# Optimization experiments

Measured on AMD Instinct MI355X. Metric: run time of the kernel, lower is better.

The kernel has to match this reference:

```python
import jax, jax.numpy as jnp
import numpy as np

B, T, D, H = 4, 4096, 1024, 16
DH = D // H
NB = T // 2 + 1  # rfft bins


def setup_inputs() -> dict:
    key = jax.random.key(0)
    ks = jax.random.split(key, 6)
    x = jax.random.normal(ks[0], (B, T, D), dtype=jnp.float32)
    # torch nn.Linear params: weight [out, in], bias [out]
    W_qkv = jax.random.normal(ks[1], (3 * D, D), dtype=jnp.float32) * 0.02
    b_qkv = jnp.zeros((3 * D,), dtype=jnp.float32)
    W_o = jax.random.normal(ks[2], (D, D), dtype=jnp.float32) * 0.02
    b_o = jnp.zeros((D,), dtype=jnp.float32)
    # per-head per-bin spectral filters (smart-init-like small values)
    log_gain = jax.random.normal(ks[3], (H, NB), dtype=jnp.float32) * 0.05
    phase = jax.random.normal(ks[4], (H, NB), dtype=jnp.float32) * 0.01
    return {"x": x, "W_qkv": W_qkv, "b_qkv": b_qkv, "W_o": W_o,
            "b_o": b_o, "log_gain": log_gain, "phase": phase}


def reference(x, W_qkv, b_qkv, W_o, b_o, log_gain, phase):
    # qkv projection; only v is used on the spectral path (q,k discarded)
    qkv = jnp.einsum('btd,ed->bte', x, W_qkv) + b_qkv  # [B,T,3D]
    v = qkv[..., 2 * D:]                               # [B,T,D]
    v = v.reshape(B, T, H, DH).transpose(0, 2, 1, 3)   # [B,H,T,DH]
    # rFFT along the token dim
    v_f = jnp.fft.rfft(v.astype(jnp.float32), axis=2)  # [B,H,NB,DH] complex
    # per-head per-bin complex filter: polar(exp(log_gain), phase)
    mag = jnp.exp(log_gain)
    comp = jax.lax.complex(mag * jnp.cos(phase), mag * jnp.sin(phase))  # [H,NB]
    v_f = v_f * comp[None, :, :, None]
    y_h = jnp.fft.irfft(v_f, n=T, axis=2)              # [B,H,T,DH]
    y = y_h.transpose(0, 2, 1, 3).reshape(B, T, D)     # [B,T,D]
    y = jnp.einsum('btd,ed->bte', y, W_o) + b_o
    return x + y
```

## Files before the change

kernel.cpp:

```cpp
#include <hip/hip_runtime.h>
#include <hip/hip_bf16.h>
#include <math.h>

#define B_BATCH 4
#define T_LEN   4096
#define D_DIM   1024
#define H_HEADS 16
#define NB_BINS 2049
#define M_ROWS  (B_BATCH * T_LEN)

typedef __attribute__((ext_vector_type(8))) short short8;
typedef __attribute__((ext_vector_type(8))) unsigned short u16x8;
typedef __attribute__((ext_vector_type(4))) float f32x4;

__device__ __forceinline__ ushort f2bf(float f) {
    unsigned b = __float_as_uint(f);
    unsigned r = (b + 0x7fffu + ((b >> 16) & 1u)) >> 16;
    return (ushort)r;
}
__device__ __forceinline__ float bf2f(ushort u) {
    return __uint_as_float(((unsigned)u) << 16);
}

__global__ void cvt_f32_to_bf16(const float* __restrict__ src, ushort* __restrict__ dst, int n4) {
    int i = blockIdx.x * 256 + threadIdx.x;
    if (i >= n4) return;
    float4 v = ((const float4*)src)[i];
    ushort4 o;
    o.x = f2bf(v.x); o.y = f2bf(v.y); o.z = f2bf(v.z); o.w = f2bf(v.w);
    ((ushort4*)dst)[i] = o;
}

__global__ void cvt_weights(const float* __restrict__ wv, const float* __restrict__ wo,
                            ushort* __restrict__ wvb, ushort* __restrict__ wob, int n4) {
    int i = blockIdx.x * 256 + threadIdx.x;
    const float* src = (i < n4) ? wv : wo;
    ushort* dst = (i < n4) ? wvb : wob;
    int j = (i < n4) ? i : (i - n4);
    float4 v = ((const float4*)src)[j];
    ushort4 o;
    o.x = f2bf(v.x); o.y = f2bf(v.y); o.z = f2bf(v.z); o.w = f2bf(v.w);
    ((ushort4*)dst)[j] = o;
}

__device__ __forceinline__ int drev16(int i) {
    return ((i & 15) << 8) | (i & 0xF0) | (i >> 8);
}

__global__ void prep_tables(const float* __restrict__ lg, const float* __restrict__ ph,
                            float2* __restrict__ Cdr, float2* __restrict__ tw) {
    int idx = blockIdx.x * 256 + threadIdx.x;
    if (idx < 4096) {
        double th = -2.0 * 3.14159265358979323846 * (double)idx / 4096.0;
        tw[idx] = make_float2((float)cos(th), (float)sin(th));
    }
    if (idx >= H_HEADS * 4096) return;
    int h = idx >> 12, i = idx & 4095;
    int f = drev16(i);
    int fc = (f <= 2048) ? f : (4096 - f);
    float sgn = (f <= 2048) ? 1.f : -1.f;
    float m = expf(lg[h * NB_BINS + fc]) * (1.0f / 4096.0f);
    float p = ph[h * NB_BINS + fc];
    float re = m * __cosf(p), im = sgn * m * __sinf(p);
    if (fc == 0 || fc == 2048) im = 0.f;
    Cdr[idx] = make_float2(re, im);
}

template<bool RESID, bool BIASROW>
__global__ __launch_bounds__(512, 1) void gemm256(const ushort* __restrict__ A,
        const ushort* __restrict__ Bm, const float* __restrict__ bias,
        const float* __restrict__ resid, void* __restrict__ Cout,
        int M, int N, int K) {
    __shared__ ushort lds[49152];
    const int tid  = threadIdx.x;
    const int lane = tid & 63;
    const int wid  = tid >> 6;
    const int wr   = wid >> 2, wc = wid & 3;
    const int fr   = lane & 15;
    const int nbn  = N >> 8;
    int bid = (int)blockIdx.x;
    bid = (bid & 7) * ((int)gridDim.x >> 3) + (bid >> 3);
    const int bm = bid / nbn, bn = bid % nbn;
    const int row0 = bm << 8, col0 = bn << 8;
    const int NT = K >> 5;

    f32x4 acc[8][4];
#pragma unroll
    for (int i = 0; i < 8; i++)
#pragma unroll
        for (int j = 0; j < 4; j++) acc[i][j] = (f32x4){0.f, 0.f, 0.f, 0.f};

    auto stage = [&](const ushort* P, int gr0, int k0, int lb) {
#pragma unroll
        for (int i = 0; i < 2; i++) {
            int r = (wid << 5) + (i << 4) + (lane >> 2);
            int c = ((lane & 3) ^ ((lane >> 3) & 3)) << 3;
            const ushort* g = P + (size_t)(gr0 + r) * (size_t)K + (size_t)(k0 + c);
            __builtin_amdgcn_global_load_lds(
                (const __attribute__((address_space(1))) void*)g,
                (__attribute__((address_space(3))) void*)&lds[lb + (((wid << 1) + i) << 9)],
                16, 0, 0);
        }
    };
    auto rdfrag = [&](int base, int row) -> short8 {
        int g = (((lane >> 4) ^ ((row >> 1) & 3)) << 3);
        return *(const short8*)&lds[base + (row << 5) + g];
    };

    stage(A,  row0, 0, 0);
    stage(Bm, col0, 0, 24576);
    stage(A,  row0, 32, 8192);
    stage(Bm, col0, 32, 24576 + 8192);
    asm volatile("s_waitcnt vmcnt(4)" ::: "memory");
    __builtin_amdgcn_sched_barrier(0);
    __builtin_amdgcn_s_barrier();

    short8 aF[4], bF[4];
    for (int t = 0; t < NT; ++t) {
        const int cb = (t % 3) << 13;
        const int sb = ((t + 2) % 3) << 13;
        const bool st = (t + 2) < NT;
        const int k2 = (t + 2) << 5;

#pragma unroll
        for (int mi = 0; mi < 4; mi++) aF[mi] = rdfrag(cb, (wr << 7) + (mi << 4) + fr);
#pragma unroll
        for (int ni = 0; ni < 4; ni++) bF[ni] = rdfrag(24576 + cb, (wc << 6) + (ni << 4) + fr);
        if (st) stage(A, row0, k2, sb);
        __builtin_amdgcn_s_barrier();
        asm volatile("s_waitcnt lgkmcnt(0)" ::: "memory");
        __builtin_amdgcn_sched_barrier(0);
        __builtin_amdgcn_s_setprio(1);
#pragma unroll
        for (int mi = 0; mi < 4; mi++)
#pragma unroll
            for (int ni = 0; ni < 4; ni++)
                acc[mi][ni] = __builtin_amdgcn_mfma_f32_16x16x32_bf16(aF[mi], bF[ni], acc[mi][ni], 0, 0, 0);
        __builtin_amdgcn_s_setprio(0);
        __builtin_amdgcn_sched_barrier(0);
        __builtin_amdgcn_s_barrier();

#pragma unroll
        for (int mi = 0; mi < 4; mi++) aF[mi] = rdfrag(cb, (wr << 7) + 64 + (mi << 4) + fr);
        if (st) stage(Bm, col0, k2, 24576 + sb);
        __builtin_amdgcn_s_barrier();
        asm volatile("s_waitcnt lgkmcnt(0)" ::: "memory");
        __builtin_amdgcn_sched_barrier(0);
        __builtin_amdgcn_s_setprio(1);
#pragma unroll
        for (int mi = 0; mi < 4; mi++)
#pragma unroll
            for (int ni = 0; ni < 4; ni++)
                acc[4 + mi][ni] = __builtin_amdgcn_mfma_f32_16x16x32_bf16(aF[mi], bF[ni], acc[4 + mi][ni], 0, 0, 0);
        __builtin_amdgcn_s_setprio(0);
        __builtin_amdgcn_sched_barrier(0);
        if (t + 1 < NT) {
            if (st) asm volatile("s_waitcnt vmcnt(4)" ::: "memory");
            else    asm volatile("s_waitcnt vmcnt(0)" ::: "memory");
        }
        __builtin_amdgcn_s_barrier();
    }

    const int crow = (lane >> 4) << 2;
#pragma unroll
    for (int mi = 0; mi < 8; mi++) {
#pragma unroll
        for (int ni = 0; ni < 4; ni++) {
            int row = row0 + (wr << 7) + (mi << 4) + crow;
            int col = col0 + (wc << 6) + (ni << 4) + fr;
            float bcol = BIASROW ? 0.f : bias[col];
#pragma unroll
            for (int j = 0; j < 4; j++) {
                float v = acc[mi][ni][j] + (BIASROW ? bias[row + j] : bcol);
                size_t off = (size_t)(row + j) * N + col;
                if (RESID) ((float*)Cout)[off] = resid[off] + v;
                else       ((ushort*)Cout)[off] = f2bf(v);
            }
        }
    }
}

__device__ __forceinline__ float2 cadd(float2 a, float2 b){ return make_float2(a.x+b.x, a.y+b.y); }
__device__ __forceinline__ float2 csub(float2 a, float2 b){ return make_float2(a.x-b.x, a.y-b.y); }
__device__ __forceinline__ float2 jmulp(float2 z){ return make_float2(-z.y, z.x); }
__device__ __forceinline__ float2 cmul(float2 a, float2 b){
    return make_float2(fmaf(a.x,b.x,-a.y*b.y), fmaf(a.x,b.y, a.y*b.x)); }
__device__ __forceinline__ float2 cmulc(float2 a, float2 b){
    return make_float2(fmaf(a.x,b.x, a.y*b.y), fmaf(a.y,b.x,-a.x*b.y)); }

template<int INV>
__device__ __forceinline__ void bf4(float2& a, float2& b, float2& c, float2& d) {
    float2 acp = cadd(a,c), acm = csub(a,c);
    float2 bdp = cadd(b,d), bdm = csub(b,d);
    float2 jb  = jmulp(bdm);
    a = cadd(acp, bdp);
    c = csub(acp, bdp);
    if (INV) { b = cadd(acm, jb); d = csub(acm, jb); }
    else     { b = csub(acm, jb); d = cadd(acm, jb); }
}

#define C16_1 0.9238795325112867f
#define S16_1 0.3826834323650898f
#define R16_2 0.7071067811865476f

template<int INV>
__device__ __forceinline__ void dft16(float2 v[16]) {
    const float sg = INV ? 1.f : -1.f;
    bf4<INV>(v[0], v[4], v[8],  v[12]);
    bf4<INV>(v[1], v[5], v[9],  v[13]);
    bf4<INV>(v[2], v[6], v[10], v[14]);
    bf4<INV>(v[3], v[7], v[11], v[15]);
    const float2 w1 = make_float2( C16_1, sg*S16_1);
    const float2 w2 = make_float2( R16_2, sg*R16_2);
    const float2 w3 = make_float2( S16_1, sg*C16_1);
    const float2 w6 = make_float2(-R16_2, sg*R16_2);
    const float2 w9 = make_float2(-C16_1,-sg*S16_1);
    v[5]  = cmul(v[5],  w1);
    v[6]  = cmul(v[6],  w2);
    v[7]  = cmul(v[7],  w3);
    v[9]  = cmul(v[9],  w2);
    v[10] = INV ? jmulp(v[10]) : make_float2(v[10].y, -v[10].x);
    v[11] = cmul(v[11], w6);
    v[13] = cmul(v[13], w3);
    v[14] = cmul(v[14], w6);
    v[15] = cmul(v[15], w9);
    bf4<INV>(v[0],  v[1],  v[2],  v[3]);
    bf4<INV>(v[4],  v[5],  v[6],  v[7]);
    bf4<INV>(v[8],  v[9],  v[10], v[11]);
    bf4<INV>(v[12], v[13], v[14], v[15]);
}

__host__ __device__ constexpr int oidx(int r) { return ((r & 3) << 2) | (r >> 2); }

template<int INV>
__device__ __forceinline__ void dft16p(float2 v[16]) {
    const float sg = INV ? 1.f : -1.f;
    bf4<INV>(v[oidx(0)], v[oidx(4)], v[oidx(8)],  v[oidx(12)]);
    bf4<INV>(v[oidx(1)], v[oidx(5)], v[oidx(9)],  v[oidx(13)]);
    bf4<INV>(v[oidx(2)], v[oidx(6)], v[oidx(10)], v[oidx(14)]);
    bf4<INV>(v[oidx(3)], v[oidx(7)], v[oidx(11)], v[oidx(15)]);
    const float2 w1 = make_float2( C16_1, sg*S16_1);
    const float2 w2 = make_float2( R16_2, sg*R16_2);
    const float2 w3 = make_float2( S16_1, sg*C16_1);
    const float2 w6 = make_float2(-R16_2, sg*R16_2);
    const float2 w9 = make_float2(-C16_1,-sg*S16_1);
    v[oidx(5)]  = cmul(v[oidx(5)],  w1);
    v[oidx(6)]  = cmul(v[oidx(6)],  w2);
    v[oidx(7)]  = cmul(v[oidx(7)],  w3);
    v[oidx(9)]  = cmul(v[oidx(9)],  w2);
    v[oidx(10)] = INV ? jmulp(v[oidx(10)]) : make_float2(v[oidx(10)].y, -v[oidx(10)].x);
    v[oidx(11)] = cmul(v[oidx(11)], w6);
    v[oidx(13)] = cmul(v[oidx(13)], w3);
    v[oidx(14)] = cmul(v[oidx(14)], w6);
    v[oidx(15)] = cmul(v[oidx(15)], w9);
    bf4<INV>(v[oidx(0)],  v[oidx(1)],  v[oidx(2)],  v[oidx(3)]);
    bf4<INV>(v[oidx(4)],  v[oidx(5)],  v[oidx(6)],  v[oidx(7)]);
    bf4<INV>(v[oidx(8)],  v[oidx(9)],  v[oidx(10)], v[oidx(11)]);
    bf4<INV>(v[oidx(12)], v[oidx(13)], v[oidx(14)], v[oidx(15)]);
}

__device__ __forceinline__ int phz(int t) { return t ^ (((t >> 4) ^ (t >> 8)) & 15); }

template<typename F>
__device__ __forceinline__ void tw_powers(float2 w1, F&& apply) {
    apply(1, w1);
    float2 w2 = cmul(w1, w1);   apply(2, w2);
    float2 w3 = cmul(w2, w1);   apply(3, w3);
    float2 w4 = cmul(w2, w2);   apply(4, w4);
    float2 w5 = cmul(w4, w1);   apply(5, w5);
    float2 w6 = cmul(w4, w2);   apply(6, w6);
    float2 w7 = cmul(w4, w3);   apply(7, w7);
    float2 w8 = cmul(w4, w4);   apply(8, w8);
    apply(9,  cmul(w8, w1));
    apply(10, cmul(w8, w2));
    apply(11, cmul(w8, w3));
    apply(12, cmul(w8, w4));
    apply(13, cmul(w8, w5));
    apply(14, cmul(w8, w6));
    apply(15, cmul(w8, w7));
}

__global__ __launch_bounds__(256) void fft16_filter(const ushort* __restrict__ VT,
                                                    ushort* __restrict__ yT,
                                                    const float2* __restrict__ tw,
                                                    const float2* __restrict__ Cdr) {
    __shared__ float2 X[2][4096];
    const int tid = threadIdx.x;
    const int b   = blockIdx.x >> 8;
    const int qb  = blockIdx.x & 255;
    const int d0  = qb << 2;
    const int h   = qb >> 4;

    float2 v[2][16];
#pragma unroll
    for (int p = 0; p < 2; p++) {
        const ushort* sRe = VT + (size_t)(d0 + 2 * p) * M_ROWS + b * T_LEN;
        const ushort* sIm = VT + (size_t)(d0 + 2 * p + 1) * M_ROWS + b * T_LEN;
#pragma unroll
        for (int j = 0; j < 16; j++)
            v[p][j] = make_float2(bf2f(sRe[tid + (j << 8)]), bf2f(sIm[tid + (j << 8)]));
    }

    dft16<0>(v[0]);
    dft16<0>(v[1]);
    {
        float2 w1 = tw[tid];
        tw_powers(w1, [&](int r, float2 w) {
            v[0][oidx(r)] = cmul(v[0][oidx(r)], w);
            v[1][oidx(r)] = cmul(v[1][oidx(r)], w);
        });
    }
#pragma unroll
    for (int r = 0; r < 16; r++) {
        int a = phz(tid + (r << 8));
        X[0][a] = v[0][oidx(r)];
        X[1][a] = v[1][oidx(r)];
    }
    __syncthreads();

    const int p2 = tid & 15, g2 = tid >> 4;
    const int base2 = (g2 << 8) + p2;
#pragma unroll
    for (int j = 0; j < 16; j++) {
        int a = phz(base2 + (j << 4));
        v[0][j] = X[0][a];
        v[1][j] = X[1][a];
    }
    dft16<0>(v[0]);
    dft16<0>(v[1]);
#pragma unroll
    for (int r = 1; r < 16; r++) {
        float2 w = tw[(p2 * r) << 4];
        v[0][oidx(r)] = cmul(v[0][oidx(r)], w);
        v[1][oidx(r)] = cmul(v[1][oidx(r)], w);
    }
#pragma unroll
    for (int r = 0; r < 16; r++) {
        int a = phz(base2 + (r << 4));
        X[0][a] = v[0][oidx(r)];
        X[1][a] = v[1][oidx(r)];
    }
    __syncthreads();

    const int base3 = tid << 4;
#pragma unroll
    for (int j = 0; j < 16; j++) {
        int a = phz(base3 + j);
        v[0][j] = X[0][a];
        v[1][j] = X[1][a];
    }
    dft16<0>(v[0]);
    dft16<0>(v[1]);
    const float2* Ch = Cdr + (h << 12) + base3;
#pragma unroll
    for (int r = 0; r < 16; r++) {
        float2 c = Ch[r];
        v[0][oidx(r)] = cmul(v[0][oidx(r)], c);
        v[1][oidx(r)] = cmul(v[1][oidx(r)], c);
    }
    dft16p<1>(v[0]);
    dft16p<1>(v[1]);
#pragma unroll
    for (int r = 0; r < 16; r++) {
        int a = phz(base3 + r);
        X[0][a] = v[0][r];
        X[1][a] = v[1][r];
    }
    __syncthreads();

#pragma unroll
    for (int j = 0; j < 16; j++) {
        int a = phz(base2 + (j << 4));
        v[0][j] = X[0][a];
        v[1][j] = X[1][a];
    }
#pragma unroll
    for (int j = 1; j < 16; j++) {
        float2 w = tw[(p2 * j) << 4];
        v[0][j] = cmulc(v[0][j], w);
        v[1][j] = cmulc(v[1][j], w);
    }
    dft16<1>(v[0]);
    dft16<1>(v[1]);
#pragma unroll
    for (int r = 0; r < 16; r++) {
        int a = phz(base2 + (r << 4));
        X[0][a] = v[0][oidx(r)];
        X[1][a] = v[1][oidx(r)];
    }
    __syncthreads();

#pragma unroll
    for (int j = 0; j < 16; j++) {
        int a = phz(tid + (j << 8));
        v[0][j] = X[0][a];
        v[1][j] = X[1][a];
    }
    {
        float2 w1 = tw[tid];
        tw_powers(w1, [&](int r, float2 w) {
            v[0][r] = cmulc(v[0][r], w);
            v[1][r] = cmulc(v[1][r], w);
        });
    }
    dft16<1>(v[0]);
    dft16<1>(v[1]);
#pragma unroll
    for (int p = 0; p < 2; p++) {
        ushort* dRe = yT + (size_t)(d0 + 2 * p) * M_ROWS + b * T_LEN;
        ushort* dIm = yT + (size_t)(d0 + 2 * p + 1) * M_ROWS + b * T_LEN;
#pragma unroll
        for (int r = 0; r < 16; r++) {
            float2 val = v[p][oidx(r)];
            dRe[tid + (r << 8)] = f2bf(val.x);
            dIm[tid + (r << 8)] = f2bf(val.y);
        }
    }
}

__global__ __launch_bounds__(256) void transpose_yT(const ushort* __restrict__ src,
                                                    ushort* __restrict__ dst) {
    __shared__ ushort tile[4096];
    const int tid = threadIdx.x;
    const int bm = blockIdx.x & 255;
    const int bd = blockIdx.x >> 8;
    const int m0 = bm << 6, d0 = bd << 6;
#pragma unroll
    for (int i = 0; i < 2; i++) {
        int vn = tid + (i << 8);
        int r  = vn >> 3;
        int c8 = (vn & 7) << 3;
        u16x8 val = *(const u16x8*)&src[(size_t)(d0 + r) * M_ROWS + m0 + c8];
#pragma unroll
        for (int q = 0; q < 8; q++)
            tile[(r << 6) | ((c8 + q) ^ r)] = (ushort)val[q];
    }
    __syncthreads();
    const int dc = tid & 63;
    const int wb = tid >> 6;
#pragma unroll
    for (int i = 0; i < 16; i++) {
        int mr = wb + (i << 2);
        dst[(size_t)(m0 + mr) * D_DIM + d0 + dc] = tile[(dc << 6) | (mr ^ dc)];
    }
}

extern "C" void kernel_launch(void* const* d_in, const int* in_sizes, int n_in,
                              void* d_out, int out_size, void* d_ws, size_t ws_size,
                              hipStream_t stream) {
    const float* x    = (const float*)d_in[0];
    const float* Wqkv = (const float*)d_in[1];
    const float* bqkv = (const float*)d_in[2];
    const float* Wo   = (const float*)d_in[3];
    const float* bo   = (const float*)d_in[4];
    const float* lg   = (const float*)d_in[5];
    const float* ph   = (const float*)d_in[6];

    char* ws = (char*)d_ws;
    ushort* xb  = (ushort*)ws;
    ushort* Wvb = (ushort*)(ws + 33554432);
    ushort* Wob = (ushort*)(ws + 35651584);
    float2* tw  = (float2*)(ws + 37748736);
    float2* Cdr = (float2*)(ws + 37781504);

    ushort* VT   = (ushort*)d_out;
    ushort* yT   = (ushort*)((char*)d_out + 33554432);
    ushort* ynat = xb;
    float*  out  = (float*)d_out;

    prep_tables<<<(H_HEADS * 4096) / 256, 256, 0, stream>>>(lg, ph, Cdr, tw);
    cvt_f32_to_bf16<<<(16777216 / 4) / 256, 256, 0, stream>>>(x, xb, 16777216 / 4);
    cvt_weights<<<2 * (1048576 / 4) / 256, 256, 0, stream>>>(
        Wqkv + 2048 * 1024, Wo, Wvb, Wob, 1048576 / 4);

    gemm256<false, true><<<(D_DIM / 256) * (M_ROWS / 256), 512, 0, stream>>>(
        Wvb, xb, bqkv + 2 * D_DIM, nullptr, (void*)VT, D_DIM, M_ROWS, D_DIM);

    fft16_filter<<<B_BATCH * (D_DIM / 4), 256, 0, stream>>>(VT, yT, tw, Cdr);

    transpose_yT<<<(M_ROWS / 64) * (D_DIM / 64), 256, 0, stream>>>(yT, ynat);

    gemm256<true, false><<<(M_ROWS / 256) * (D_DIM / 256), 512, 0, stream>>>(
        ynat, Wob, bo, x, (void*)out, M_ROWS, D_DIM, D_DIM);
}
```

Before: 165.8 us.

## Restructure GEMM mainloop to 64-wide K steps with double-buffered sub-stages

The bf16 GEMM pipeline moves from a triple-buffered 32-wide K loop to a double-buffered loop that handles two 32-wide sub-tiles per iteration, so each iteration processes 64 of K. LDS grows to 128KB, and the A and B loads for later sub-stages are spread across four compute phases with adjusted vmcnt waits. The aim is to reduce per-iteration loop and barrier overhead and keep more loads in flight. The cost is higher LDS use and more complex wait-count logic that has to stay correct at the edges.

```diff
diff --git a/kernel.cpp b/kernel.cpp
--- a/kernel.cpp
+++ b/kernel.cpp
@@ -71,7 +71,7 @@
         const ushort* __restrict__ Bm, const float* __restrict__ bias,
         const float* __restrict__ resid, void* __restrict__ Cout,
         int M, int N, int K) {
-    __shared__ ushort lds[49152];
+    __shared__ ushort lds[65536];
     const int tid  = threadIdx.x;
     const int lane = tid & 63;
     const int wid  = tid >> 6;
@@ -82,7 +82,7 @@
     bid = (bid & 7) * ((int)gridDim.x >> 3) + (bid >> 3);
     const int bm = bid / nbn, bn = bid % nbn;
     const int row0 = bm << 8, col0 = bn << 8;
-    const int NT = K >> 5;
+    const int NT = K >> 6;
 
     f32x4 acc[8][4];
 #pragma unroll
@@ -90,15 +90,31 @@
 #pragma unroll
         for (int j = 0; j < 4; j++) acc[i][j] = (f32x4){0.f, 0.f, 0.f, 0.f};
 
-    auto stage = [&](const ushort* P, int gr0, int k0, int lb) {
+    auto stageA = [&](int t, int s) {
+        int base = (((t & 1) << 1) + s) << 13;
+        int k0 = (t << 6) + (s << 5);
 #pragma unroll
         for (int i = 0; i < 2; i++) {
             int r = (wid << 5) + (i << 4) + (lane >> 2);
             int c = ((lane & 3) ^ ((lane >> 3) & 3)) << 3;
-            const ushort* g = P + (size_t)(gr0 + r) * (size_t)K + (size_t)(k0 + c);
+            const ushort* g = A + (size_t)(row0 + r) * (size_t)K + (size_t)(k0 + c);
             __builtin_amdgcn_global_load_lds(
                 (const __attribute__((address_space(1))) void*)g,
-                (__attribute__((address_space(3))) void*)&lds[lb + (((wid << 1) + i) << 9)],
+                (__attribute__((address_space(3))) void*)&lds[base + (((wid << 1) + i) << 9)],
+                16, 0, 0);
+        }
+    };
+    auto stageB = [&](int t, int s) {
+        int base = 32768 + ((((t & 1) << 1) + s) << 13);
+        int k0 = (t << 6) + (s << 5);
+#pragma unroll
+        for (int i = 0; i < 2; i++) {
+            int r = (wid << 5) + (i << 4) + (lane >> 2);
+            int c = ((lane & 3) ^ ((lane >> 3) & 3)) << 3;
+            const ushort* g = Bm + (size_t)(col0 + r) * (size_t)K + (size_t)(k0 + c);
+            __builtin_amdgcn_global_load_lds(
+                (const __attribute__((address_space(1))) void*)g,
+                (__attribute__((address_space(3))) void*)&lds[base + (((wid << 1) + i) << 9)],
                 16, 0, 0);
         }
     };
@@ -107,26 +123,28 @@
         return *(const short8*)&lds[base + (row << 5) + g];
     };
 
-    stage(A,  row0, 0, 0);
-    stage(Bm, col0, 0, 24576);
-    stage(A,  row0, 32, 8192);
-    stage(Bm, col0, 32, 24576 + 8192);
-    asm volatile("s_waitcnt vmcnt(4)" ::: "memory");
+    stageA(0, 0); stageA(0, 1); stageB(0, 0); stageB(0, 1);
+    if (NT > 1) stageA(1, 0);
+    if (NT > 1) asm volatile("s_waitcnt vmcnt(4)" ::: "memory");
+    else        asm volatile("s_waitcnt vmcnt(2)" ::: "memory");
     __builtin_amdgcn_sched_barrier(0);
     __builtin_amdgcn_s_barrier();
 
     short8 aF[4], bF[4];
     for (int t = 0; t < NT; ++t) {
-        const int cb = (t % 3) << 13;
-        const int sb = ((t + 2) % 3) << 13;
-        const bool st = (t + 2) < NT;
-        const int k2 = (t + 2) << 5;
-
-#pragma unroll
-        for (int mi = 0; mi < 4; mi++) aF[mi] = rdfrag(cb, (wr << 7) + (mi << 4) + fr);
-#pragma unroll
-        for (int ni = 0; ni < 4; ni++) bF[ni] = rdfrag(24576 + cb, (wc << 6) + (ni << 4) + fr);
-        if (st) stage(A, row0, k2, sb);
+        const int d  = t & 1;
+        const int ab0 = ((d << 1) + 0) << 13;
+        const int ab1 = ((d << 1) + 1) << 13;
+        const int bb0 = 32768 + (((d << 1) + 0) << 13);
+        const int bb1 = 32768 + (((d << 1) + 1) << 13);
+        const bool st1 = (t + 1) < NT;
+        const bool st2 = (t + 2) < NT;
+
+#pragma unroll
+        for (int mi = 0; mi < 4; mi++) aF[mi] = rdfrag(ab0, (wr << 7) + (mi << 4) + fr);
+#pragma unroll
+        for (int ni = 0; ni < 4; ni++) bF[ni] = rdfrag(bb0, (wc << 6) + (ni << 4) + fr);
+        if (st1) stageA(t + 1, 1);
         __builtin_amdgcn_s_barrier();
         asm volatile("s_waitcnt lgkmcnt(0)" ::: "memory");
         __builtin_amdgcn_sched_barrier(0);
@@ -141,8 +159,8 @@
         __builtin_amdgcn_s_barrier();
 
 #pragma unroll
-        for (int mi = 0; mi < 4; mi++) aF[mi] = rdfrag(cb, (wr << 7) + 64 + (mi << 4) + fr);
-        if (st) stage(Bm, col0, k2, 24576 + sb);
+        for (int mi = 0; mi < 4; mi++) aF[mi] = rdfrag(ab0, (wr << 7) + 64 + (mi << 4) + fr);
+        if (st1) stageB(t + 1, 0);
         __builtin_amdgcn_s_barrier();
         asm volatile("s_waitcnt lgkmcnt(0)" ::: "memory");
         __builtin_amdgcn_sched_barrier(0);
@@ -154,10 +172,45 @@
                 acc[4 + mi][ni] = __builtin_amdgcn_mfma_f32_16x16x32_bf16(aF[mi], bF[ni], acc[4 + mi][ni], 0, 0, 0);
         __builtin_amdgcn_s_setprio(0);
         __builtin_amdgcn_sched_barrier(0);
-        if (t + 1 < NT) {
-            if (st) asm volatile("s_waitcnt vmcnt(4)" ::: "memory");
-            else    asm volatile("s_waitcnt vmcnt(0)" ::: "memory");
-        }
+        if (st1) asm volatile("s_waitcnt vmcnt(4)" ::: "memory");
+        else     asm volatile("s_waitcnt vmcnt(0)" ::: "memory");
+        __builtin_amdgcn_s_barrier();
+
+#pragma unroll
+        for (int mi = 0; mi < 4; mi++) aF[mi] = rdfrag(ab1, (wr << 7) + (mi << 4) + fr);
+#pragma unroll
+        for (int ni = 0; ni < 4; ni++) bF[ni] = rdfrag(bb1, (wc << 6) + (ni << 4) + fr);
+        if (st2) stageA(t + 2, 0);
+        __builtin_amdgcn_s_barrier();
+        asm volatile("s_waitcnt lgkmcnt(0)" ::: "memory");
+        __builtin_amdgcn_sched_barrier(0);
+        __builtin_amdgcn_s_setprio(1);
+#pragma unroll
+        for (int mi = 0; mi < 4; mi++)
+#pragma unroll
+            for (int ni = 0; ni < 4; ni++)
+                acc[mi][ni] = __builtin_amdgcn_mfma_f32_16x16x32_bf16(aF[mi], bF[ni], acc[mi][ni], 0, 0, 0);
+        __builtin_amdgcn_s_setprio(0);
+        __builtin_amdgcn_sched_barrier(0);
+        __builtin_amdgcn_s_barrier();
+
+#pragma unroll
+        for (int mi = 0; mi < 4; mi++) aF[mi] = rdfrag(ab1, (wr << 7) + 64 + (mi << 4) + fr);
+        if (st1) stageB(t + 1, 1);
+        __builtin_amdgcn_s_barrier();
+        asm volatile("s_waitcnt lgkmcnt(0)" ::: "memory");
+        __builtin_amdgcn_sched_barrier(0);
+        __builtin_amdgcn_s_setprio(1);
+#pragma unroll
+        for (int mi = 0; mi < 4; mi++)
+#pragma unroll
+            for (int ni = 0; ni < 4; ni++)
+                acc[4 + mi][ni] = __builtin_amdgcn_mfma_f32_16x16x32_bf16(aF[mi], bF[ni], acc[4 + mi][ni], 0, 0, 0);
+        __builtin_amdgcn_s_setprio(0);
+        __builtin_amdgcn_sched_barrier(0);
+        if (st2)      asm volatile("s_waitcnt vmcnt(4)" ::: "memory");
+        else if (st1) asm volatile("s_waitcnt vmcnt(2)" ::: "memory");
+        else          asm volatile("s_waitcnt vmcnt(0)" ::: "memory");
         __builtin_amdgcn_s_barrier();
     }
 
```

Measured after the change: 164.9 us. About the same (-0.5%).

## Replace triple-buffered 32-wide K pipeline with double-buffered 64-wide K steps

Applied to the files above, without the earlier changes.

Rewrites the GEMM main loop from a 3-stage ring of K=32 tiles, with hand-placed barriers, waitcnts and setprio, into a 2-stage double buffer of K=64 tiles (LDS grows to 128KB) with one __syncthreads per iteration. This halves the number of loop iterations and barriers. It drops the explicit vmcnt waits, setprio and sched_barrier interleaving, relying on __syncthreads to wait for the global_load_lds data. That may serialize the loads with compute and lose overlap. It also raises LDS use to the full 128KB per block.

```diff
diff --git a/kernel.cpp b/kernel.cpp
--- a/kernel.cpp
+++ b/kernel.cpp
@@ -71,7 +71,7 @@
         const ushort* __restrict__ Bm, const float* __restrict__ bias,
         const float* __restrict__ resid, void* __restrict__ Cout,
         int M, int N, int K) {
-    __shared__ ushort lds[49152];
+    __shared__ ushort lds[65536];
     const int tid  = threadIdx.x;
     const int lane = tid & 63;
     const int wid  = tid >> 6;
@@ -82,7 +82,7 @@
     bid = (bid & 7) * ((int)gridDim.x >> 3) + (bid >> 3);
     const int bm = bid / nbn, bn = bid % nbn;
     const int row0 = bm << 8, col0 = bn << 8;
-    const int NT = K >> 5;
+    const int NT = K >> 6;
 
     f32x4 acc[8][4];
 #pragma unroll
@@ -90,15 +90,31 @@
 #pragma unroll
         for (int j = 0; j < 4; j++) acc[i][j] = (f32x4){0.f, 0.f, 0.f, 0.f};
 
-    auto stage = [&](const ushort* P, int gr0, int k0, int lb) {
+    auto stageA = [&](int t, int s) {
+        int base = (((t & 1) << 1) + s) << 13;
+        int k0 = (t << 6) + (s << 5);
 #pragma unroll
         for (int i = 0; i < 2; i++) {
             int r = (wid << 5) + (i << 4) + (lane >> 2);
             int c = ((lane & 3) ^ ((lane >> 3) & 3)) << 3;
-            const ushort* g = P + (size_t)(gr0 + r) * (size_t)K + (size_t)(k0 + c);
+            const ushort* g = A + (size_t)(row0 + r) * (size_t)K + (size_t)(k0 + c);
             __builtin_amdgcn_global_load_lds(
                 (const __attribute__((address_space(1))) void*)g,
-                (__attribute__((address_space(3))) void*)&lds[lb + (((wid << 1) + i) << 9)],
+                (__attribute__((address_space(3))) void*)&lds[base + (((wid << 1) + i) << 9)],
+                16, 0, 0);
+        }
+    };
+    auto stageB = [&](int t, int s) {
+        int base = 32768 + ((((t & 1) << 1) + s) << 13);
+        int k0 = (t << 6) + (s << 5);
+#pragma unroll
+        for (int i = 0; i < 2; i++) {
+            int r = (wid << 5) + (i << 4) + (lane >> 2);
+            int c = ((lane & 3) ^ ((lane >> 3) & 3)) << 3;
+            const ushort* g = Bm + (size_t)(col0 + r) * (size_t)K + (size_t)(k0 + c);
+            __builtin_amdgcn_global_load_lds(
+                (const __attribute__((address_space(1))) void*)g,
+                (__attribute__((address_space(3))) void*)&lds[base + (((wid << 1) + i) << 9)],
                 16, 0, 0);
         }
     };
@@ -107,58 +123,36 @@
         return *(const short8*)&lds[base + (row << 5) + g];
     };
 
-    stage(A,  row0, 0, 0);
-    stage(Bm, col0, 0, 24576);
-    stage(A,  row0, 32, 8192);
-    stage(Bm, col0, 32, 24576 + 8192);
-    asm volatile("s_waitcnt vmcnt(4)" ::: "memory");
-    __builtin_amdgcn_sched_barrier(0);
-    __builtin_amdgcn_s_barrier();
-
-    short8 aF[4], bF[4];
+    stageA(0, 0); stageA(0, 1); stageB(0, 0); stageB(0, 1);
+    __syncthreads();
+
     for (int t = 0; t < NT; ++t) {
-        const int cb = (t % 3) << 13;
-        const int sb = ((t + 2) % 3) << 13;
-        const bool st = (t + 2) < NT;
-        const int k2 = (t + 2) << 5;
-
-#pragma unroll
-        for (int mi = 0; mi < 4; mi++) aF[mi] = rdfrag(cb, (wr << 7) + (mi << 4) + fr);
-#pragma unroll
-        for (int ni = 0; ni < 4; ni++) bF[ni] = rdfrag(24576 + cb, (wc << 6) + (ni << 4) + fr);
-        if (st) stage(A, row0, k2, sb);
-        __builtin_amdgcn_s_barrier();
-        asm volatile("s_waitcnt lgkmcnt(0)" ::: "memory");
-        __builtin_amdgcn_sched_barrier(0);
-        __builtin_amdgcn_s_setprio(1);
-#pragma unroll
-        for (int mi = 0; mi < 4; mi++)
-#pragma unroll
-            for (int ni = 0; ni < 4; ni++)
-                acc[mi][ni] = __builtin_amdgcn_mfma_f32_16x16x32_bf16(aF[mi], bF[ni], acc[mi][ni], 0, 0, 0);
-        __builtin_amdgcn_s_setprio(0);
-        __builtin_amdgcn_sched_barrier(0);
-        __builtin_amdgcn_s_barrier();
-
-#pragma unroll
-        for (int mi = 0; mi < 4; mi++) aF[mi] = rdfrag(cb, (wr << 7) + 64 + (mi << 4) + fr);
-        if (st) stage(Bm, col0, k2, 24576 + sb);
-        __builtin_amdgcn_s_barrier();
-        asm volatile("s_waitcnt lgkmcnt(0)" ::: "memory");
-        __builtin_amdgcn_sched_barrier(0);
-        __builtin_amdgcn_s_setprio(1);
-#pragma unroll
-        for (int mi = 0; mi < 4; mi++)
-#pragma unroll
-            for (int ni = 0; ni < 4; ni++)
-                acc[4 + mi][ni] = __builtin_amdgcn_mfma_f32_16x16x32_bf16(aF[mi], bF[ni], acc[4 + mi][ni], 0, 0, 0);
-        __builtin_amdgcn_s_setprio(0);
-        __builtin_amdgcn_sched_barrier(0);
+        const int d = t & 1;
         if (t + 1 < NT) {
-            if (st) asm volatile("s_waitcnt vmcnt(4)" ::: "memory");
-            else    asm volatile("s_waitcnt vmcnt(0)" ::: "memory");
-        }
-        __builtin_amdgcn_s_barrier();
+            stageA(t + 1, 0); stageA(t + 1, 1);
+            stageB(t + 1, 0); stageB(t + 1, 1);
+        }
+#pragma unroll
+        for (int ks = 0; ks < 2; ks++) {
+            const int ab = (((d << 1) + ks) << 13);
+            const int bb = 32768 + (((d << 1) + ks) << 13);
+            short8 bF[4], aF[4];
+#pragma unroll
+            for (int ni = 0; ni < 4; ni++) bF[ni] = rdfrag(bb, (wc << 6) + (ni << 4) + fr);
+#pragma unroll
+            for (int mh = 0; mh < 2; mh++) {
+#pragma unroll
+                for (int mi = 0; mi < 4; mi++)
+                    aF[mi] = rdfrag(ab, (wr << 7) + (mh << 6) + (mi << 4) + fr);
+#pragma unroll
+                for (int mi = 0; mi < 4; mi++)
+#pragma unroll
+                    for (int ni = 0; ni < 4; ni++)
+                        acc[(mh << 2) + mi][ni] = __builtin_amdgcn_mfma_f32_16x16x32_bf16(
+                            aF[mi], bF[ni], acc[(mh << 2) + mi][ni], 0, 0, 0);
+            }
+        }
+        __syncthreads();
     }
 
     const int crow = (lane >> 4) << 2;
```

Result: no change. 163.1 us (-1.6%).
